# Kernel optimization log

Hardware: AMD Instinct MI355X
Metric: run time of the kernel (lower is better)

The kernel has to match this reference:

```python
import jax, jax.numpy as jnp
import numpy as np
import math

D_MODEL = 1024
N_HEAD = 16
D_FF = 4096
B, T, S = 2, 2048, 2048
LN_EPS = 1e-5


def _linear(x, w, b):
    # torch nn.Linear: y = x @ W.T + b, W: [out, in]
    return jnp.einsum('bsd,od->bso', x, w) + b


def _layer_norm(x, g, b):
    mu = jnp.mean(x, axis=-1, keepdims=True)
    var = jnp.var(x, axis=-1, keepdims=True)
    return (x - mu) * jax.lax.rsqrt(var + LN_EPS) * g + b


def _mha(xq, xkv, wq, bq, wk, bk, wv, bv, wo, bo, mask):
    Bq, Tq, D = xq.shape
    Tk = xkv.shape[1]
    dk = D // N_HEAD
    q = _linear(xq, wq, bq).reshape(Bq, Tq, N_HEAD, dk).transpose(0, 2, 1, 3)
    k = _linear(xkv, wk, bk).reshape(Bq, Tk, N_HEAD, dk).transpose(0, 2, 1, 3)
    v = _linear(xkv, wv, bv).reshape(Bq, Tk, N_HEAD, dk).transpose(0, 2, 1, 3)
    scores = jnp.einsum('bhqd,bhkd->bhqk', q, k) / math.sqrt(dk)
    if mask is not None:
        scores = jnp.where(mask == 0, jnp.asarray(-1e9, scores.dtype), scores)
    attn = jax.nn.softmax(scores, axis=-1)  # dropout is eval-mode identity
    out = jnp.einsum('bhqk,bhkd->bhqd', attn, v)
    out = out.transpose(0, 2, 1, 3).reshape(Bq, Tq, D)
    return _linear(out, wo, bo)


def setup_inputs() -> dict:
    key = jax.random.key(0)
    ks = jax.random.split(key, 20)
    sd = 0.02

    def w(k, shape):
        return (jax.random.normal(k, shape, dtype=jnp.float32) * sd)

    inp = {
        'x': jax.random.normal(ks[0], (B, T, D_MODEL), dtype=jnp.float32),
        'enc_output': jax.random.normal(ks[1], (B, S, D_MODEL), dtype=jnp.float32),
        # causal (future) mask for self-attention
        'tgt_mask': jnp.tril(jnp.ones((T, T), dtype=jnp.int32))[None, None, :, :].repeat(B, axis=0),
        # no source padding -> all ones
        'src_tgt_mask': jnp.ones((B, 1, T, S), dtype=jnp.int32),
        'sa_wq': w(ks[2], (D_MODEL, D_MODEL)), 'sa_bq': jnp.zeros((D_MODEL,), jnp.float32),
        'sa_wk': w(ks[3], (D_MODEL, D_MODEL)), 'sa_bk': jnp.zeros((D_MODEL,), jnp.float32),
        'sa_wv': w(ks[4], (D_MODEL, D_MODEL)), 'sa_bv': jnp.zeros((D_MODEL,), jnp.float32),
        'sa_wo': w(ks[5], (D_MODEL, D_MODEL)), 'sa_bo': jnp.zeros((D_MODEL,), jnp.float32),
        'ca_wq': w(ks[6], (D_MODEL, D_MODEL)), 'ca_bq': jnp.zeros((D_MODEL,), jnp.float32),
        'ca_wk': w(ks[7], (D_MODEL, D_MODEL)), 'ca_bk': jnp.zeros((D_MODEL,), jnp.float32),
        'ca_wv': w(ks[8], (D_MODEL, D_MODEL)), 'ca_bv': jnp.zeros((D_MODEL,), jnp.float32),
        'ca_wo': w(ks[9], (D_MODEL, D_MODEL)), 'ca_bo': jnp.zeros((D_MODEL,), jnp.float32),
        'ffn_w1': w(ks[10], (D_FF, D_MODEL)), 'ffn_b1': jnp.zeros((D_FF,), jnp.float32),
        'ffn_w2': w(ks[11], (D_MODEL, D_FF)), 'ffn_b2': jnp.zeros((D_MODEL,), jnp.float32),
        'ln1_g': jnp.ones((D_MODEL,), jnp.float32), 'ln1_b': jnp.zeros((D_MODEL,), jnp.float32),
        'ln2_g': jnp.ones((D_MODEL,), jnp.float32), 'ln2_b': jnp.zeros((D_MODEL,), jnp.float32),
        'ln3_g': jnp.ones((D_MODEL,), jnp.float32), 'ln3_b': jnp.zeros((D_MODEL,), jnp.float32),
    }
    return inp


def reference(x, enc_output, tgt_mask, src_tgt_mask,
              sa_wq, sa_bq, sa_wk, sa_bk, sa_wv, sa_bv, sa_wo, sa_bo,
              ca_wq, ca_bq, ca_wk, ca_bk, ca_wv, ca_bv, ca_wo, ca_bo,
              ffn_w1, ffn_b1, ffn_w2, ffn_b2,
              ln1_g, ln1_b, ln2_g, ln2_b, ln3_g, ln3_b):
    # masked self-attention + residual + LN
    a1 = _mha(x, x, sa_wq, sa_bq, sa_wk, sa_bk, sa_wv, sa_bv, sa_wo, sa_bo, tgt_mask)
    x = _layer_norm(x + a1, ln1_g, ln1_b)
    # cross-attention + residual + LN
    a2 = _mha(x, enc_output, ca_wq, ca_bq, ca_wk, ca_bk, ca_wv, ca_bv, ca_wo, ca_bo, src_tgt_mask)
    x = _layer_norm(x + a2, ln2_g, ln2_b)
    # FFN + residual + LN
    h = jax.nn.relu(_linear(x, ffn_w1, ffn_b1))
    f = _linear(h, ffn_w2, ffn_b2)
    x = _layer_norm(x + f, ln3_g, ln3_b)
    return x
```

## Files before the change

kernel.cpp:

```cpp
#include <hip/hip_runtime.h>
#include <stdint.h>

typedef uint16_t u16;
typedef __attribute__((ext_vector_type(8))) short short8;
typedef __attribute__((ext_vector_type(4))) short short4v;
typedef __attribute__((ext_vector_type(4))) float f32x4;
typedef __attribute__((ext_vector_type(2))) unsigned int u32x2;

#define GLB_AS __attribute__((address_space(1)))
#define LDS_AS __attribute__((address_space(3)))

__device__ __forceinline__ void gload_lds16(const void* g, void* l) {
  __builtin_amdgcn_global_load_lds((GLB_AS void*)(g), (LDS_AS void*)(l), 16, 0, 0);
}

__device__ __forceinline__ float bf2f(u16 u) {
  union { uint32_t i; float f; } v; v.i = ((uint32_t)u) << 16; return v.f;
}
__device__ __forceinline__ u16 f2bf(float f) {
  uint32_t x = __builtin_bit_cast(uint32_t, f);
  return (u16)((x + 0x7fffu + ((x >> 16) & 1u)) >> 16);
}
__device__ __forceinline__ uint32_t cvtpk(float lo, float hi) {
  uint32_t r;
  asm("v_cvt_pk_bf16_f32 %0, %1, %2" : "=v"(r) : "v"(lo), "v"(hi));
  return r;
}

struct CastJobs {
  const float* s[12];
  u16* d[12];
  int n[12];
};
__global__ __launch_bounds__(256) void cast_many(CastJobs j)
{
  const int job = blockIdx.y;
  const int i = (blockIdx.x * 256 + threadIdx.x) * 4;
  if (i >= j.n[job]) return;
  const float4 v = *(const float4*)(j.s[job] + i);
  short4v r;
  r[0] = (short)f2bf(v.x); r[1] = (short)f2bf(v.y);
  r[2] = (short)f2bf(v.z); r[3] = (short)f2bf(v.w);
  *(short4v*)(j.d[job] + i) = r;
}

__global__ __launch_bounds__(256) void vtrans(
    const u16* __restrict__ V, int vs, u16* __restrict__ Vt)
{
  __shared__ u16 tl[64][72];
  const int tid = threadIdx.x;
  const int b = blockIdx.z, h = blockIdx.y, t0 = blockIdx.x * 64;
#pragma unroll
  for (int it = 0; it < 2; ++it) {
    const int r = (tid >> 3) + it*32, c = (tid & 7) * 8;
    short8 vv = *(const short8*)(V + (size_t)(b*2048 + t0 + r)*vs + h*64 + c);
    *(short8*)(&tl[r][c]) = vv;
  }
  __syncthreads();
#pragma unroll
  for (int it = 0; it < 2; ++it) {
    const int d = (tid >> 3) + it*32, t8 = (tid & 7) * 8;
    short8 ov;
#pragma unroll
    for (int j = 0; j < 8; ++j) ov[j] = (short)tl[t8 + j][d];
    *(short8*)(Vt + ((size_t)((b*16 + h)*64 + d))*2048 + t0 + t8) = ov;
  }
}

template<int RELU, int NSEG, int BN>
__global__ __launch_bounds__(256) void gemm_bt(
    const u16* __restrict__ A, const u16* __restrict__ W,
    const float* __restrict__ b0, const float* __restrict__ b1,
    const float* __restrict__ b2, u16* __restrict__ Y,
    int M, int N, int K)
{
  __shared__ __attribute__((aligned(16))) u16 lA[2][128*64];
  __shared__ __attribute__((aligned(16))) u16 lB[2][BN*64];
  const int tid  = threadIdx.x;
  const int lane = tid & 63, wv = tid >> 6;
  constexpr int WM = (BN == 128) ? 64 : 32;
  constexpr int MI = WM / 16;
  constexpr int BRND = BN / 32;
  const int wm = (BN == 128) ? (wv >> 1) : wv;
  const int wn = (BN == 128) ? (wv & 1) : 0;
  const int l16 = lane & 15, l4 = lane >> 4;
  const int rswz = (l16 & 7) << 4;

  const int gx = gridDim.x;
  int flat = blockIdx.y * gx + blockIdx.x;
  flat = (flat & 7) * ((gx * gridDim.y) >> 3) + (flat >> 3);
  const int bx = (flat % gx) * BN, by = (flat / gx) * 128;

  const f32x4 fzero = {0.f, 0.f, 0.f, 0.f};
  f32x4 acc[MI][4];
#pragma unroll
  for (int i = 0; i < MI; ++i)
#pragma unroll
    for (int j = 0; j < 4; ++j) acc[i][j] = fzero;

  const int o = wv*1024 + lane*16;

  auto stage = [&](int k0, int buf) {
#pragma unroll
    for (int r = 0; r < 4; ++r) {
      const int oo = r*4096 + o;
      const int row = oo >> 7;
      const int src = ((oo & 127) ^ ((row & 7) << 4)) >> 1;
      gload_lds16(A + (size_t)(by + row)*K + (k0 + src), (char*)lA[buf] + oo);
    }
#pragma unroll
    for (int r = 0; r < BRND; ++r) {
      const int oo = r*4096 + o;
      const int row = oo >> 7;
      const int src = ((oo & 127) ^ ((row & 7) << 4)) >> 1;
      gload_lds16(W + (size_t)(bx + row)*K + (k0 + src), (char*)lB[buf] + oo);
    }
  };

  stage(0, 0);
  const int KT = K >> 6;
  for (int kt = 0; kt < KT; ++kt) {
    const int cur = kt & 1;
    __syncthreads();
    short8 af[2][MI], bfv[2][4];
#pragma unroll
    for (int ks = 0; ks < 2; ++ks) {
      const int cb = (ks*64 + l4*16) ^ rswz;
#pragma unroll
      for (int i = 0; i < MI; ++i)
        af[ks][i]  = *(const short8*)((const char*)lA[cur] + (wm*WM + i*16 + l16)*128 + cb);
#pragma unroll
      for (int j = 0; j < 4; ++j)
        bfv[ks][j] = *(const short8*)((const char*)lB[cur] + (wn*64 + j*16 + l16)*128 + cb);
    }
    if (kt + 1 < KT) stage((kt + 1) << 6, cur ^ 1);
#pragma unroll
    for (int ks = 0; ks < 2; ++ks)
#pragma unroll
      for (int i = 0; i < MI; ++i)
#pragma unroll
        for (int j = 0; j < 4; ++j)
          acc[i][j] = __builtin_amdgcn_mfma_f32_16x16x32_bf16(af[ks][i], bfv[ks][j], acc[i][j], 0, 0, 0);
  }

#pragma unroll
  for (int j = 0; j < 4; ++j) {
    const int col = bx + wn*64 + j*16 + l16;
    float bv;
    if (NSEG == 1) bv = b0[col];
    else {
      const int seg = col >> 10, off = col & 1023;
      const float* bp = (seg == 0) ? b0 : ((seg == 1) ? b1 : b2);
      bv = bp[off];
    }
#pragma unroll
    for (int i = 0; i < MI; ++i) {
      const int r0 = by + wm*WM + i*16 + l4*4;
#pragma unroll
      for (int r = 0; r < 4; ++r) {
        float v = acc[i][j][r] + bv;
        if (RELU) v = v > 0.f ? v : 0.f;
        Y[(size_t)(r0 + r)*N + col] = f2bf(v);
      }
    }
  }
}

template<int CAUSAL, int QR>
__global__ __launch_bounds__(512, (QR == 16) ? 4 : 2) void attn_fwd(
    const u16* __restrict__ Q, int qs,
    const u16* __restrict__ K, int ks_,
    const u16* __restrict__ Vt, u16* __restrict__ O, int Tk)
{
  constexpr int NG = QR / 16;
  __shared__ __attribute__((aligned(16))) u16 lK[2][128*64];
  __shared__ __attribute__((aligned(16))) u16 lV[2][64*128];
  __shared__ __attribute__((aligned(16))) u16 lP[8][NG*1024];
  const int tid  = threadIdx.x;
  const int lane = tid & 63, wv = tid >> 6;
  const int l16 = lane & 15, l4 = lane >> 4;
  const int b = blockIdx.z, h = blockIdx.y;
  int strip;
  if (CAUSAL) {
    const int u = (blockIdx.x + blockIdx.z) & 15;
    strip = (u & 1) ? (15 - (u >> 1)) : (u >> 1);
  } else {
    strip = blockIdx.x;
  }
  const int Bq = strip * (8 * QR);
  const int qrow = Bq + wv*QR;

  short8 qf[NG][2];
#pragma unroll
  for (int g = 0; g < NG; ++g) {
    const u16* Qb = Q + (size_t)(b*2048 + qrow + g*16 + l16)*qs + h*64;
#pragma unroll
    for (int ks = 0; ks < 2; ++ks)
      qf[g][ks] = *(const short8*)(Qb + ks*32 + l4*8);
  }

  const f32x4 fzero = {0.f, 0.f, 0.f, 0.f};
  f32x4 accO[NG][4];
#pragma unroll
  for (int g = 0; g < NG; ++g)
#pragma unroll
    for (int i = 0; i < 4; ++i) accO[g][i] = fzero;
  float lrow[NG];
#pragma unroll
  for (int g = 0; g < NG; ++g) lrow[g] = 0.f;

  const int kend = CAUSAL ? (Bq + 8*QR) : Tk;
  const int nt = kend >> 7;
  const int qmax = qrow + QR - 1;
  const int srK = tid >> 3;
  const int scK = 8 * ((tid & 7) ^ (srK & 7));
  const int srV = tid >> 4;
  const int scV = 8 * ((tid & 15) ^ (srV & 7));
  const u16* KbG = K  + (size_t)(b*2048)*ks_ + h*64 + scK;
  const u16* VbG = Vt + ((size_t)((b*16 + h)*64 + srV))*2048 + scV;
  const int wvoff = (tid >> 6) * 1024;
  const int rswz = (l16 & 7) << 4;
  const float SCL = 0.18033688f;
  const int sbq = (lane & 48) + l4*4;

  char* const pbuf = (char*)lP + (tid >> 6) * (NG*2048);
  const int swzP = (l16 & 7) << 4;
  int wrA[4], rdA[2];
#pragma unroll
  for (int nf = 0; nf < 4; ++nf) wrA[nf] = l16*128 + ((nf*32 + l4*8) ^ swzP);
#pragma unroll
  for (int c = 0; c < 2; ++c)    rdA[c] = l16*128 + ((c*64 + l4*16) ^ swzP);

  auto readK = [&](int h2, int bb, short8 (&kf)[4][2]) {
#pragma unroll
    for (int nf = 0; nf < 4; ++nf) {
      const char* base = (const char*)lK[bb] + (h2*64 + nf*16 + l16)*128;
      kf[nf][0] = *(const short8*)(base + ((l4*16)      ^ rswz));
      kf[nf][1] = *(const short8*)(base + ((64 + l4*16) ^ rswz));
    }
  };

  auto compute64 = [&](int h2, int kvb, short8 (&kf)[4][2], int bb) {
#pragma unroll
    for (int g = 0; g < NG; ++g) {
      f32x4 sf[4];
      __builtin_amdgcn_s_setprio(1);
#pragma unroll
      for (int nf = 0; nf < 4; ++nf) {
        f32x4 s = fzero;
        s = __builtin_amdgcn_mfma_f32_16x16x32_bf16(kf[nf][0], qf[g][0], s, 0, 0, 0);
        s = __builtin_amdgcn_mfma_f32_16x16x32_bf16(kf[nf][1], qf[g][1], s, 0, 0, 0);
        sf[nf] = s;
      }
      __builtin_amdgcn_s_setprio(0);
      if (CAUSAL && (kvb + 63 > qrow + g*16)) {
        const int q = qrow + g*16 + l16;
#pragma unroll
        for (int nf = 0; nf < 4; ++nf)
#pragma unroll
          for (int r = 0; r < 4; ++r) {
            const int kv = kvb + nf*16 + l4*4 + r;
            if (kv > q) sf[nf][r] = -1e30f;
          }
      }
#pragma unroll
      for (int nf = 0; nf < 4; ++nf)
#pragma unroll
        for (int r = 0; r < 4; ++r)
          sf[nf][r] = exp2f(sf[nf][r] * SCL);
      float sm[4];
#pragma unroll
      for (int nf = 0; nf < 4; ++nf)
        sm[nf] = (sf[nf][0] + sf[nf][1]) + (sf[nf][2] + sf[nf][3]);
      lrow[g] += (sm[0] + sm[1]) + (sm[2] + sm[3]);
#pragma unroll
      for (int nf = 0; nf < 4; ++nf) {
        u32x2 w;
        w[0] = cvtpk(sf[nf][0], sf[nf][1]);
        w[1] = cvtpk(sf[nf][2], sf[nf][3]);
        *(u32x2*)(pbuf + g*2048 + wrA[nf]) = w;
      }
    }
#pragma unroll
    for (int c = 0; c < 2; ++c) {
      short8 pa[NG];
#pragma unroll
      for (int g = 0; g < NG; ++g)
        pa[g] = *(const short8*)(pbuf + g*2048 + rdA[c]);
      __builtin_amdgcn_s_setprio(1);
#pragma unroll
      for (int df = 0; df < 4; ++df) {
        const short8 vf = *(const short8*)((const char*)lV[bb] +
            (df*16 + l16)*256 + ((h2*128 + c*64 + l4*16) ^ rswz));
#pragma unroll
        for (int g = 0; g < NG; ++g)
          accO[g][df] = __builtin_amdgcn_mfma_f32_16x16x32_bf16(pa[g], vf, accO[g][df], 0, 0, 0);
      }
      __builtin_amdgcn_s_setprio(0);
    }
  };

#pragma unroll
  for (int r = 0; r < 2; ++r) {
    gload_lds16(KbG + (size_t)(r*64 + srK)*ks_, (char*)lK[0] + r*8192 + wvoff);
    gload_lds16(VbG + (size_t)(r*32)*2048,      (char*)lV[0] + r*8192 + wvoff);
  }

  for (int t = 0; t < nt; ++t) {
    const int bb = t & 1;
    const int kb = t << 7;
    __syncthreads();
    short8 kf[4][2];
    readK(0, bb, kf);
    if (t + 1 < nt) {
      const int kb2 = kb + 128;
#pragma unroll
      for (int r = 0; r < 2; ++r) {
        gload_lds16(KbG + (size_t)(kb2 + r*64 + srK)*ks_,
                    (char*)lK[bb^1] + r*8192 + wvoff);
        gload_lds16(VbG + (size_t)(r*32)*2048 + kb2,
                    (char*)lV[bb^1] + r*8192 + wvoff);
      }
    }
    compute64(0, kb, kf, bb);
    if (!CAUSAL || (kb + 64 <= qmax)) {
      readK(1, bb, kf);
      compute64(1, kb + 64, kf, bb);
    }
  }

#pragma unroll
  for (int g = 0; g < NG; ++g) {
    lrow[g] += __shfl_xor(lrow[g], 16);
    lrow[g] += __shfl_xor(lrow[g], 32);
    u16* Ob = O + (size_t)(b*2048 + qrow + g*16 + l4*4)*1024 + h*64;
#pragma unroll
    for (int r = 0; r < 4; ++r) {
      const float inv = 1.f / __shfl(lrow[g], sbq + r);
#pragma unroll
      for (int df = 0; df < 4; ++df)
        Ob[(size_t)r*1024 + df*16 + l16] = f2bf(accO[g][df][r] * inv);
    }
  }
}

template<int XF32, int OF32>
__global__ __launch_bounds__(256) void add_ln(
    const void* __restrict__ Xp, const u16* __restrict__ R,
    const float* __restrict__ G, const float* __restrict__ Bb,
    void* __restrict__ OUTp)
{
  const int row = blockIdx.x;
  const int tid = threadIdx.x;
  const size_t base = (size_t)row*1024 + tid*4;
  float xv[4];
  if (XF32) {
    const float4 t = *(const float4*)((const float*)Xp + base);
    xv[0] = t.x; xv[1] = t.y; xv[2] = t.z; xv[3] = t.w;
  } else {
    short4v t = *(const short4v*)((const u16*)Xp + base);
#pragma unroll
    for (int i = 0; i < 4; ++i) xv[i] = bf2f((u16)t[i]);
  }
  short4v rv = *(const short4v*)(R + base);
  float v[4], s = 0.f, s2 = 0.f;
#pragma unroll
  for (int i = 0; i < 4; ++i) {
    float t = xv[i] + bf2f((u16)rv[i]);
    v[i] = t; s += t; s2 += t*t;
  }
#pragma unroll
  for (int m = 1; m < 64; m <<= 1) { s += __shfl_xor(s, m); s2 += __shfl_xor(s2, m); }
  __shared__ float red[8];
  const int w = tid >> 6, lane = tid & 63;
  if (lane == 0) { red[w] = s; red[4 + w] = s2; }
  __syncthreads();
  s  = red[0] + red[1] + red[2] + red[3];
  s2 = red[4] + red[5] + red[6] + red[7];
  const float mu  = s * (1.f/1024.f);
  const float var = s2 * (1.f/1024.f) - mu*mu;
  const float rs  = rsqrtf(var + 1e-5f);
  if (OF32) {
    float4 ov;
    ov.x = (v[0]-mu)*rs*G[tid*4+0] + Bb[tid*4+0];
    ov.y = (v[1]-mu)*rs*G[tid*4+1] + Bb[tid*4+1];
    ov.z = (v[2]-mu)*rs*G[tid*4+2] + Bb[tid*4+2];
    ov.w = (v[3]-mu)*rs*G[tid*4+3] + Bb[tid*4+3];
    *(float4*)((float*)OUTp + base) = ov;
  } else {
    short4v ov;
#pragma unroll
    for (int i = 0; i < 4; ++i)
      ov[i] = (short)f2bf((v[i] - mu)*rs*G[tid*4+i] + Bb[tid*4+i]);
    *(short4v*)((u16*)OUTp + base) = ov;
  }
}

extern "C" void kernel_launch(void* const* d_in, const int* in_sizes, int n_in,
                              void* d_out, int out_size, void* d_ws, size_t ws_size,
                              hipStream_t stream)
{
  (void)in_sizes; (void)n_in; (void)out_size; (void)ws_size;
  const float* x    = (const float*)d_in[0];
  const float* enc  = (const float*)d_in[1];
  const float* sa_wq = (const float*)d_in[4];  const float* sa_bq = (const float*)d_in[5];
  const float* sa_wk = (const float*)d_in[6];  const float* sa_bk = (const float*)d_in[7];
  const float* sa_wv = (const float*)d_in[8];  const float* sa_bv = (const float*)d_in[9];
  const float* sa_wo = (const float*)d_in[10]; const float* sa_bo = (const float*)d_in[11];
  const float* ca_wq = (const float*)d_in[12]; const float* ca_bq = (const float*)d_in[13];
  const float* ca_wk = (const float*)d_in[14]; const float* ca_bk = (const float*)d_in[15];
  const float* ca_wv = (const float*)d_in[16]; const float* ca_bv = (const float*)d_in[17];
  const float* ca_wo = (const float*)d_in[18]; const float* ca_bo = (const float*)d_in[19];
  const float* w1 = (const float*)d_in[20];    const float* b1 = (const float*)d_in[21];
  const float* w2 = (const float*)d_in[22];    const float* b2 = (const float*)d_in[23];
  const float* ln1g = (const float*)d_in[24];  const float* ln1b = (const float*)d_in[25];
  const float* ln2g = (const float*)d_in[26];  const float* ln2b = (const float*)d_in[27];
  const float* ln3g = (const float*)d_in[28];  const float* ln3b = (const float*)d_in[29];
  float* out = (float*)d_out;

  char* ws = (char*)d_ws;
  const size_t MB = 1024*1024;
  u16* xb   = (u16*)(ws);
  u16* encb = (u16*)(ws + 8*MB);
  u16* wsab = (u16*)(ws + 16*MB);
  u16* wcab = (u16*)(ws + 24*MB);
  u16* x1   = (u16*)(ws + 32*MB);
  u16* ao   = (u16*)(ws + 40*MB);
  u16* tmp  = (u16*)(ws + 48*MB);
  u16* vt   = (u16*)(ws + 56*MB);
  u16* qkv  = (u16*)(ws + 64*MB);
  u16* kvb  = (u16*)(ws + 88*MB);
  u16* x2   = xb;
  u16* hb   = qkv;
  u16* w1b  = encb;
  u16* w2b  = vt;

  const int NW = 1024*1024;
  const int NX = 4096*1024;
  dim3 blk(256);

  {
    CastJobs cj{};
    cj.s[0] = x;     cj.d[0] = xb;           cj.n[0] = NX;
    cj.s[1] = enc;   cj.d[1] = encb;         cj.n[1] = NX;
    cj.s[2] = sa_wq; cj.d[2] = wsab + 0*NW;  cj.n[2] = NW;
    cj.s[3] = sa_wk; cj.d[3] = wsab + 1*NW;  cj.n[3] = NW;
    cj.s[4] = sa_wv; cj.d[4] = wsab + 2*NW;  cj.n[4] = NW;
    cj.s[5] = sa_wo; cj.d[5] = wsab + 3*NW;  cj.n[5] = NW;
    cj.s[6] = ca_wq; cj.d[6] = wcab + 0*NW;  cj.n[6] = NW;
    cj.s[7] = ca_wk; cj.d[7] = wcab + 1*NW;  cj.n[7] = NW;
    cj.s[8] = ca_wv; cj.d[8] = wcab + 2*NW;  cj.n[8] = NW;
    cj.s[9] = ca_wo; cj.d[9] = wcab + 3*NW;  cj.n[9] = NW;
    cast_many<<<dim3(NX/1024, 10), blk, 0, stream>>>(cj);
  }

  const int M = 4096;
  dim3 gN64(16, 32);
  dim3 gQKV(24, 32);
  dim3 gKV(16, 32);
  dim3 gF1(32, 32);
  dim3 gAttn(16, 16, 2);
  dim3 gT(32, 16, 2);
  dim3 blk512(512);

  gemm_bt<0,3,128><<<gQKV, blk, 0, stream>>>(xb, wsab, sa_bq, sa_bk, sa_bv, qkv, M, 3072, 1024);
  vtrans<<<gT, blk, 0, stream>>>(qkv + 2048, 3072, vt);
  attn_fwd<1,16><<<gAttn, blk512, 0, stream>>>(qkv, 3072, qkv + 1024, 3072, vt, ao, 2048);
  gemm_bt<0,1,64><<<gN64, blk, 0, stream>>>(ao, wsab + 3*NW, sa_bo, sa_bo, sa_bo, tmp, M, 1024, 1024);
  add_ln<1,0><<<4096, blk, 0, stream>>>(x, tmp, ln1g, ln1b, x1);

  gemm_bt<0,1,64><<<gN64, blk, 0, stream>>>(x1, wcab + 0*NW, ca_bq, ca_bq, ca_bq, qkv, M, 1024, 1024);
  gemm_bt<0,2,128><<<gKV, blk, 0, stream>>>(encb, wcab + 1*NW, ca_bk, ca_bv, ca_bv, kvb, M, 2048, 1024);
  vtrans<<<gT, blk, 0, stream>>>(kvb + 1024, 2048, vt);
  attn_fwd<0,16><<<gAttn, blk512, 0, stream>>>(qkv, 1024, kvb, 2048, vt, ao, 2048);
  {
    CastJobs cj{};
    cj.s[0] = w1; cj.d[0] = w1b; cj.n[0] = NX;
    cj.s[1] = w2; cj.d[1] = w2b; cj.n[1] = NX;
    cast_many<<<dim3(NX/1024, 2), blk, 0, stream>>>(cj);
  }
  gemm_bt<0,1,64><<<gN64, blk, 0, stream>>>(ao, wcab + 3*NW, ca_bo, ca_bo, ca_bo, tmp, M, 1024, 1024);
  add_ln<0,0><<<4096, blk, 0, stream>>>(x1, tmp, ln2g, ln2b, x2);

  gemm_bt<1,1,128><<<gF1, blk, 0, stream>>>(x2, w1b, b1, b1, b1, hb, M, 4096, 1024);
  gemm_bt<0,1,64><<<gN64, blk, 0, stream>>>(hb, w2b, b2, b2, b2, tmp, M, 1024, 4096);
  add_ln<0,1><<<4096, blk, 0, stream>>>(x2, tmp, ln3g, ln3b, out);
}
```

Measured before the change: 328.1 us.

## Triple-buffer BN64 GEMM, fold softmax scale into Q projection, merge FFN weight casts

The BN=64 GEMM moves to a three-buffer LDS pipeline that issues the next tile's loads before computing, with explicit vmcnt waits and a single barrier per K step, to overlap global loads with MFMA work. The softmax scale factor is applied to Q in the projection epilogue, removing a multiply per score in attention, at the cost of rounding Q to bf16 after scaling. When the workspace is large enough, the FFN weight casts are merged into the initial cast launch, removing one kernel launch. The triple buffer raises LDS use per block, which may lower occupancy.

Measured after the change: 327.7 us. No clear change (-0.1%).

```diff
diff --git a/kernel.cpp b/kernel.cpp
--- a/kernel.cpp
+++ b/kernel.cpp
@@ -67,15 +67,16 @@
   }
 }
 
-template<int RELU, int NSEG, int BN>
+template<int RELU, int NSEG, int BN, int SCALEQ>
 __global__ __launch_bounds__(256) void gemm_bt(
     const u16* __restrict__ A, const u16* __restrict__ W,
     const float* __restrict__ b0, const float* __restrict__ b1,
     const float* __restrict__ b2, u16* __restrict__ Y,
     int M, int N, int K)
 {
-  __shared__ __attribute__((aligned(16))) u16 lA[2][128*64];
-  __shared__ __attribute__((aligned(16))) u16 lB[2][BN*64];
+  constexpr int NBUF = (BN == 64) ? 3 : 2;
+  __shared__ __attribute__((aligned(16))) u16 lA[NBUF][128*64];
+  __shared__ __attribute__((aligned(16))) u16 lB[NBUF][BN*64];
   const int tid  = threadIdx.x;
   const int lane = tid & 63, wv = tid >> 6;
   constexpr int WM = (BN == 128) ? 64 : 32;
@@ -117,11 +118,7 @@
     }
   };
 
-  stage(0, 0);
-  const int KT = K >> 6;
-  for (int kt = 0; kt < KT; ++kt) {
-    const int cur = kt & 1;
-    __syncthreads();
+  auto compute = [&](int cur) {
     short8 af[2][MI], bfv[2][4];
 #pragma unroll
     for (int ks = 0; ks < 2; ++ks) {
@@ -133,7 +130,6 @@
       for (int j = 0; j < 4; ++j)
         bfv[ks][j] = *(const short8*)((const char*)lB[cur] + (wn*64 + j*16 + l16)*128 + cb);
     }
-    if (kt + 1 < KT) stage((kt + 1) << 6, cur ^ 1);
 #pragma unroll
     for (int ks = 0; ks < 2; ++ks)
 #pragma unroll
@@ -141,15 +137,62 @@
 #pragma unroll
         for (int j = 0; j < 4; ++j)
           acc[i][j] = __builtin_amdgcn_mfma_f32_16x16x32_bf16(af[ks][i], bfv[ks][j], acc[i][j], 0, 0, 0);
-  }
-
+  };
+
+  const int KT = K >> 6;
+  if constexpr (BN == 64) {
+    stage(0, 0);
+    int cur = 0;
+    for (int kt = 0; kt < KT; ++kt) {
+      const int nxt = (cur + 1 == 3) ? 0 : cur + 1;
+      if (kt + 1 < KT) {
+        stage((kt + 1) << 6, nxt);
+        asm volatile("s_waitcnt vmcnt(6)" ::: "memory");
+      } else {
+        asm volatile("s_waitcnt vmcnt(0)" ::: "memory");
+      }
+      __builtin_amdgcn_s_barrier();
+      __builtin_amdgcn_sched_barrier(0);
+      compute(cur);
+      cur = nxt;
+    }
+  } else {
+    stage(0, 0);
+    for (int kt = 0; kt < KT; ++kt) {
+      const int cur = kt & 1;
+      __syncthreads();
+      short8 af[2][MI], bfv[2][4];
+#pragma unroll
+      for (int ks = 0; ks < 2; ++ks) {
+        const int cb = (ks*64 + l4*16) ^ rswz;
+#pragma unroll
+        for (int i = 0; i < MI; ++i)
+          af[ks][i]  = *(const short8*)((const char*)lA[cur] + (wm*WM + i*16 + l16)*128 + cb);
+#pragma unroll
+        for (int j = 0; j < 4; ++j)
+          bfv[ks][j] = *(const short8*)((const char*)lB[cur] + (wn*64 + j*16 + l16)*128 + cb);
+      }
+      if (kt + 1 < KT) stage((kt + 1) << 6, cur ^ 1);
+#pragma unroll
+      for (int ks = 0; ks < 2; ++ks)
+#pragma unroll
+        for (int i = 0; i < MI; ++i)
+#pragma unroll
+          for (int j = 0; j < 4; ++j)
+            acc[i][j] = __builtin_amdgcn_mfma_f32_16x16x32_bf16(af[ks][i], bfv[ks][j], acc[i][j], 0, 0, 0);
+    }
+  }
+
+  const float SCLF = 0.18033688f;
 #pragma unroll
   for (int j = 0; j < 4; ++j) {
     const int col = bx + wn*64 + j*16 + l16;
     float bv;
+    int seg = 0;
     if (NSEG == 1) bv = b0[col];
     else {
-      const int seg = col >> 10, off = col & 1023;
+      seg = col >> 10;
+      const int off = col & 1023;
       const float* bp = (seg == 0) ? b0 : ((seg == 1) ? b1 : b2);
       bv = bp[off];
     }
@@ -160,6 +203,7 @@
       for (int r = 0; r < 4; ++r) {
         float v = acc[i][j][r] + bv;
         if (RELU) v = v > 0.f ? v : 0.f;
+        if (SCALEQ && (NSEG == 1 || seg == 0)) v *= SCLF;
         Y[(size_t)(r0 + r)*N + col] = f2bf(v);
       }
     }
@@ -220,7 +264,6 @@
   const u16* VbG = Vt + ((size_t)((b*16 + h)*64 + srV))*2048 + scV;
   const int wvoff = (tid >> 6) * 1024;
   const int rswz = (l16 & 7) << 4;
-  const float SCL = 0.18033688f;
   const int sbq = (lane & 48) + l4*4;
 
   char* const pbuf = (char*)lP + (tid >> 6) * (NG*2048);
@@ -267,7 +310,7 @@
       for (int nf = 0; nf < 4; ++nf)
 #pragma unroll
         for (int r = 0; r < 4; ++r)
-          sf[nf][r] = exp2f(sf[nf][r] * SCL);
+          sf[nf][r] = exp2f(sf[nf][r]);
       float sm[4];
 #pragma unroll
       for (int nf = 0; nf < 4; ++nf)
@@ -400,7 +443,7 @@
                               void* d_out, int out_size, void* d_ws, size_t ws_size,
                               hipStream_t stream)
 {
-  (void)in_sizes; (void)n_in; (void)out_size; (void)ws_size;
+  (void)in_sizes; (void)n_in; (void)out_size;
   const float* x    = (const float*)d_in[0];
   const float* enc  = (const float*)d_in[1];
   const float* sa_wq = (const float*)d_in[4];  const float* sa_bq = (const float*)d_in[5];
@@ -432,8 +475,10 @@
   u16* kvb  = (u16*)(ws + 88*MB);
   u16* x2   = xb;
   u16* hb   = qkv;
-  u16* w1b  = encb;
-  u16* w2b  = vt;
+
+  const bool bigws = ws_size >= (size_t)120*MB;
+  u16* w1b = bigws ? (u16*)(ws + 104*MB) : encb;
+  u16* w2b = bigws ? (u16*)(ws + 112*MB) : vt;
 
   const int NW = 1024*1024;
   const int NX = 4096*1024;
@@ -451,7 +496,13 @@
     cj.s[7] = ca_wk; cj.d[7] = wcab + 1*NW;  cj.n[7] = NW;
     cj.s[8] = ca_wv; cj.d[8] = wcab + 2*NW;  cj.n[8] = NW;
     cj.s[9] = ca_wo; cj.d[9] = wcab + 3*NW;  cj.n[9] = NW;
-    cast_many<<<dim3(NX/1024, 10), blk, 0, stream>>>(cj);
+    int njobs = 10;
+    if (bigws) {
+      cj.s[10] = w1; cj.d[10] = w1b; cj.n[10] = NX;
+      cj.s[11] = w2; cj.d[11] = w2b; cj.n[11] = NX;
+      njobs = 12;
+    }
+    cast_many<<<dim3(NX/1024, njobs), blk, 0, stream>>>(cj);
   }
 
   const int M = 4096;
@@ -463,26 +514,26 @@
   dim3 gT(32, 16, 2);
   dim3 blk512(512);
 
-  gemm_bt<0,3,128><<<gQKV, blk, 0, stream>>>(xb, wsab, sa_bq, sa_bk, sa_bv, qkv, M, 3072, 1024);
+  gemm_bt<0,3,128,1><<<gQKV, blk, 0, stream>>>(xb, wsab, sa_bq, sa_bk, sa_bv, qkv, M, 3072, 1024);
   vtrans<<<gT, blk, 0, stream>>>(qkv + 2048, 3072, vt);
   attn_fwd<1,16><<<gAttn, blk512, 0, stream>>>(qkv, 3072, qkv + 1024, 3072, vt, ao, 2048);
-  gemm_bt<0,1,64><<<gN64, blk, 0, stream>>>(ao, wsab + 3*NW, sa_bo, sa_bo, sa_bo, tmp, M, 1024, 1024);
+  gemm_bt<0,1,64,0><<<gN64, blk, 0, stream>>>(ao, wsab + 3*NW, sa_bo, sa_bo, sa_bo, tmp, M, 1024, 1024);
   add_ln<1,0><<<4096, blk, 0, stream>>>(x, tmp, ln1g, ln1b, x1);
 
-  gemm_bt<0,1,64><<<gN64, blk, 0, stream>>>(x1, wcab + 0*NW, ca_bq, ca_bq, ca_bq, qkv, M, 1024, 1024);
-  gemm_bt<0,2,128><<<gKV, blk, 0, stream>>>(encb, wcab + 1*NW, ca_bk, ca_bv, ca_bv, kvb, M, 2048, 1024);
+  gemm_bt<0,1,64,1><<<gN64, blk, 0, stream>>>(x1, wcab + 0*NW, ca_bq, ca_bq, ca_bq, qkv, M, 1024, 1024);
+  gemm_bt<0,2,128,0><<<gKV, blk, 0, stream>>>(encb, wcab + 1*NW, ca_bk, ca_bv, ca_bv, kvb, M, 2048, 1024);
   vtrans<<<gT, blk, 0, stream>>>(kvb + 1024, 2048, vt);
   attn_fwd<0,16><<<gAttn, blk512, 0, stream>>>(qkv, 1024, kvb, 2048, vt, ao, 2048);
-  {
+  if (!bigws) {
     CastJobs cj{};
     cj.s[0] = w1; cj.d[0] = w1b; cj.n[0] = NX;
     cj.s[1] = w2; cj.d[1] = w2b; cj.n[1] = NX;
     cast_many<<<dim3(NX/1024, 2), blk, 0, stream>>>(cj);
   }
-  gemm_bt<0,1,64><<<gN64, blk, 0, stream>>>(ao, wcab + 3*NW, ca_bo, ca_bo, ca_bo, tmp, M, 1024, 1024);
+  gemm_bt<0,1,64,0><<<gN64, blk, 0, stream>>>(ao, wcab + 3*NW, ca_bo, ca_bo, ca_bo, tmp, M, 1024, 1024);
   add_ln<0,0><<<4096, blk, 0, stream>>>(x1, tmp, ln2g, ln2b, x2);
 
-  gemm_bt<1,1,128><<<gF1, blk, 0, stream>>>(x2, w1b, b1, b1, b1, hb, M, 4096, 1024);
-  gemm_bt<0,1,64><<<gN64, blk, 0, stream>>>(hb, w2b, b2, b2, b2, tmp, M, 1024, 4096);
+  gemm_bt<1,1,128,0><<<gF1, blk, 0, stream>>>(x2, w1b, b1, b1, b1, hb, M, 4096, 1024);
+  gemm_bt<0,1,64,0><<<gN64, blk, 0, stream>>>(hb, w2b, b2, b2, b2, tmp, M, 1024, 4096);
   add_ln<0,1><<<4096, blk, 0, stream>>>(x2, tmp, ln3g, ln3b, out);
 }
```
